# Kernel optimization log

Hardware: AMD Instinct MI355X
Metric: run time of the kernel (lower is better)

The kernel has to match this reference:

```python
import jax, jax.numpy as jnp
import numpy as np

VOCAB, D_EMBED, D_HID = 32000, 512, 512
T, B, S = 64, 32, 256


def setup_inputs() -> dict:
    key = jax.random.key(0)
    ks = jax.random.split(key, 12)
    sE = 1.0 / np.sqrt(D_EMBED)
    sH = 1.0 / np.sqrt(D_HID)
    return {
        "x_seq": jax.random.randint(ks[0], (T, B), 0, VOCAB),
        "h": jax.random.normal(ks[1], (B, D_HID), jnp.float32),
        "c": jax.random.normal(ks[2], (B, D_HID), jnp.float32),
        "context": jax.random.normal(ks[3], (B, S, D_HID), jnp.float32),
        "emb": jax.random.normal(ks[4], (VOCAB, D_EMBED), jnp.float32),
        "W_ih": jax.random.normal(ks[5], (4 * D_HID, D_EMBED), jnp.float32) * sE,
        "W_hh": jax.random.normal(ks[6], (4 * D_HID, D_HID), jnp.float32) * sH,
        "b_ih": jax.random.normal(ks[7], (4 * D_HID,), jnp.float32) * sH,
        "b_hh": jax.random.normal(ks[8], (4 * D_HID,), jnp.float32) * sH,
        "W_attn": jax.random.normal(ks[9], (D_HID, 2 * D_HID), jnp.float32) * sH,
        "W_out": jax.random.normal(ks[10], (VOCAB, D_HID), jnp.float32) * sH,
        "b_out": jax.random.normal(ks[11], (VOCAB,), jnp.float32) * sH,
    }


def reference(x_seq, h, c, context, emb, W_ih, W_hh, b_ih, b_hh, W_attn, W_out, b_out):
    e_seq = emb[x_seq]  # [T, B, E]

    def step(carry, e):
        h, c = carry
        gates = e @ W_ih.T + b_ih + h @ W_hh.T + b_hh  # [B, 4H]
        i, f, g, o = jnp.split(gates, 4, axis=-1)       # torch LSTMCell gate order
        i, f, o = jax.nn.sigmoid(i), jax.nn.sigmoid(f), jax.nn.sigmoid(o)
        g = jnp.tanh(g)
        c = f * c + i * g
        h = o * jnp.tanh(c)
        # dot global attention
        scores = jnp.einsum('bsd,bd->bs', context, h)
        attn = jax.nn.softmax(scores, axis=1)
        wctx = jnp.einsum('bs,bsd->bd', attn, context)
        a = jnp.tanh(jnp.concatenate([h, wctx], axis=1) @ W_attn.T)
        return (h, c), a

    (hf, cf), outs = jax.lax.scan(step, (h, c), e_seq)  # outs: [T, B, H]
    logits = outs.reshape(-1, D_HID) @ W_out.T + b_out   # [T*B, V]
    logp = jax.nn.log_softmax(logits, axis=1).reshape(T, B, VOCAB)
    return logp, hf, cf
```

## Files before the change

kernel.cpp:

```cpp
#include <hip/hip_runtime.h>
#include <hip/hip_cooperative_groups.h>
#include <cstdint>
#include <cstddef>

namespace cg = cooperative_groups;

#define TT 64
#define BB 32
#define SS 256
#define DH 512
#define VV 32000
#define NROWS 2048
#define G4 2048
#define NBLK_SCAN 256
#define NLEAF 32
#define LEAF_TARGET (NBLK_SCAN / NLEAF)

typedef __attribute__((ext_vector_type(8))) short short8;
typedef __attribute__((ext_vector_type(4))) float f32x4;

__device__ __forceinline__ unsigned short f2bf(float x) {
    unsigned u = __float_as_uint(x);
    u += 0x7FFFu + ((u >> 16) & 1u);
    return (unsigned short)(u >> 16);
}
__device__ __forceinline__ float bf2f(unsigned short u) {
    return __uint_as_float((unsigned)u << 16);
}

__device__ __forceinline__ void gload_lds16(const void* g, void* l) {
    __builtin_amdgcn_global_load_lds(
        (const __attribute__((address_space(1))) unsigned int*)g,
        (__attribute__((address_space(3))) unsigned int*)l, 16, 0, 0);
}

__device__ __forceinline__ void coh_store(float* p, float v) {
    __hip_atomic_store(p, v, __ATOMIC_RELAXED, __HIP_MEMORY_SCOPE_AGENT);
}

__global__ void k_convert_bf16(const float* __restrict__ src,
                               unsigned short* __restrict__ dst, int n4) {
    int i = blockIdx.x * blockDim.x + threadIdx.x;
    int stride = gridDim.x * blockDim.x;
    for (; i < n4; i += stride) {
        float4 v = ((const float4*)src)[i];
        ushort4 o;
        o.x = f2bf(v.x); o.y = f2bf(v.y); o.z = f2bf(v.z); o.w = f2bf(v.w);
        ((ushort4*)dst)[i] = o;
    }
}

__global__ void k_convert_hl(const float* __restrict__ src,
                             unsigned short* __restrict__ hi,
                             unsigned short* __restrict__ lo, int n4) {
    int i = blockIdx.x * blockDim.x + threadIdx.x;
    int stride = gridDim.x * blockDim.x;
    for (; i < n4; i += stride) {
        float4 v = ((const float4*)src)[i];
        ushort4 oh, ol;
        float f[4] = {v.x, v.y, v.z, v.w};
        unsigned short h[4], l[4];
#pragma unroll
        for (int e = 0; e < 4; ++e) {
            h[e] = f2bf(f[e]);
            l[e] = f2bf(f[e] - bf2f(h[e]));
        }
        oh.x = h[0]; oh.y = h[1]; oh.z = h[2]; oh.w = h[3];
        ol.x = l[0]; ol.y = l[1]; ol.z = l[2]; ol.w = l[3];
        ((ushort4*)hi)[i] = oh;
        ((ushort4*)lo)[i] = ol;
    }
}

__global__ void k_gather_embed_hl(const int* __restrict__ xseq,
                                  const float* __restrict__ emb,
                                  unsigned short* __restrict__ ehi,
                                  unsigned short* __restrict__ elo,
                                  int* __restrict__ cnt) {
    int gi = blockIdx.x * blockDim.x + threadIdx.x;
    if (gi < TT * NLEAF * 16) cnt[gi] = 0;
    int r = blockIdx.x;
    int tok = xseq[r];
    const float4* s = (const float4*)(emb + (size_t)tok * DH);
    ushort4* dh = (ushort4*)(ehi + (size_t)r * DH);
    ushort4* dl = (ushort4*)(elo + (size_t)r * DH);
    for (int i = threadIdx.x; i < DH / 4; i += blockDim.x) {
        float4 v = s[i];
        float f[4] = {v.x, v.y, v.z, v.w};
        unsigned short h[4], l[4];
#pragma unroll
        for (int e = 0; e < 4; ++e) {
            h[e] = f2bf(f[e]);
            l[e] = f2bf(f[e] - bf2f(h[e]));
        }
        dh[i] = make_ushort4(h[0], h[1], h[2], h[3]);
        dl[i] = make_ushort4(l[0], l[1], l[2], l[3]);
    }
}

__global__ __launch_bounds__(256)
void k_mfma_xpart(const unsigned short* __restrict__ Ahi, const unsigned short* __restrict__ Alo,
                  const unsigned short* __restrict__ Bhi, const unsigned short* __restrict__ Blo,
                  int M, int N, int K,
                  const float* __restrict__ b1, const float* __restrict__ b2,
                  float* __restrict__ Ct) {
    __shared__ unsigned short Ah_s[128 * 64];
    __shared__ unsigned short Al_s[128 * 64];
    __shared__ unsigned short Bh_s[128 * 64];
    __shared__ unsigned short Bl_s[128 * 64];

    const int tid = threadIdx.x;
    const int lane = tid & 63;
    const int wid = tid >> 6;
    const int wm = wid >> 1, wn = wid & 1;
    const int mrow0 = blockIdx.y * 128;
    const int ncol0 = blockIdx.x * 128;
    const int lr = lane & 15;
    const int lk = (lane >> 4) * 8;
    const int rw = (lane >> 4) * 4;

    f32x4 acc[4][4] = {};

    for (int kt = 0; kt < K; kt += 64) {
#pragma unroll
        for (int it = 0; it < 4; ++it) {
            int chunk = it * 256 + tid;
            int r = chunk >> 3;
            int c = (chunk & 7) * 8;
            size_t goA = (size_t)(mrow0 + r) * K + kt + c;
            size_t goB = (size_t)(ncol0 + r) * K + kt + c;
            gload_lds16(Ahi + goA, (void*)(Ah_s + chunk * 8));
            gload_lds16(Alo + goA, (void*)(Al_s + chunk * 8));
            gload_lds16(Bhi + goB, (void*)(Bh_s + chunk * 8));
            gload_lds16(Blo + goB, (void*)(Bl_s + chunk * 8));
        }
        __syncthreads();
#pragma unroll
        for (int kk = 0; kk < 2; ++kk) {
            short8 ah[4], al[4], bh[4], bl[4];
#pragma unroll
            for (int i = 0; i < 4; ++i) {
                int offA = (wm * 64 + i * 16 + lr) * 64 + kk * 32 + lk;
                int offB = (wn * 64 + i * 16 + lr) * 64 + kk * 32 + lk;
                ah[i] = *(const short8*)&Ah_s[offA];
                al[i] = *(const short8*)&Al_s[offA];
                bh[i] = *(const short8*)&Bh_s[offB];
                bl[i] = *(const short8*)&Bl_s[offB];
            }
#pragma unroll
            for (int mi = 0; mi < 4; ++mi)
#pragma unroll
                for (int ni = 0; ni < 4; ++ni) {
                    acc[mi][ni] = __builtin_amdgcn_mfma_f32_16x16x32_bf16(
                        ah[mi], bh[ni], acc[mi][ni], 0, 0, 0);
                    acc[mi][ni] = __builtin_amdgcn_mfma_f32_16x16x32_bf16(
                        ah[mi], bl[ni], acc[mi][ni], 0, 0, 0);
                    acc[mi][ni] = __builtin_amdgcn_mfma_f32_16x16x32_bf16(
                        al[mi], bh[ni], acc[mi][ni], 0, 0, 0);
                }
        }
        __syncthreads();
    }

#pragma unroll
    for (int ni = 0; ni < 4; ++ni) {
        int col = ncol0 + wn * 64 + ni * 16 + lr;
        float bs = b1[col] + b2[col];
#pragma unroll
        for (int mi = 0; mi < 4; ++mi) {
            int grow0 = mrow0 + wm * 64 + mi * 16 + rw;
            float4 o;
            o.x = acc[mi][ni][0] + bs;
            o.y = acc[mi][ni][1] + bs;
            o.z = acc[mi][ni][2] + bs;
            o.w = acc[mi][ni][3] + bs;
            *(float4*)&Ct[(size_t)col * M + grow0] = o;
        }
    }
}

template <int EPI>
__global__ __launch_bounds__(256)
void k_mfma_gemm(const unsigned short* __restrict__ A,
                 const unsigned short* __restrict__ B,
                 int M, int N, int K,
                 const float* __restrict__ bias,
                 float* __restrict__ Cf,
                 unsigned short* __restrict__ Cbf,
                 float* __restrict__ pm, float* __restrict__ ps) {
    __shared__ unsigned short A_s[128 * 64];
    __shared__ unsigned short B_s[128 * 64];
    __shared__ float part_m[2][128];
    __shared__ float part_s[2][128];

    const int tid = threadIdx.x;
    const int lane = tid & 63;
    const int wid = tid >> 6;
    const int wm = wid >> 1, wn = wid & 1;
    const int mrow0 = blockIdx.y * 128;
    const int ncol0 = blockIdx.x * 128;
    const int lr = lane & 15;
    const int lk = (lane >> 4) * 8;
    const int rw = (lane >> 4) * 4;

    f32x4 acc[4][4] = {};

    for (int kt = 0; kt < K; kt += 64) {
#pragma unroll
        for (int it = 0; it < 4; ++it) {
            int chunk = it * 256 + tid;
            int r = chunk >> 3;
            int c = (chunk & 7) * 8;
            gload_lds16(A + (size_t)(mrow0 + r) * K + kt + c, (void*)(A_s + chunk * 8));
            gload_lds16(B + (size_t)(ncol0 + r) * K + kt + c, (void*)(B_s + chunk * 8));
        }
        __syncthreads();
#pragma unroll
        for (int kk = 0; kk < 2; ++kk) {
            short8 afr[4], bfr[4];
#pragma unroll
            for (int i = 0; i < 4; ++i) {
                afr[i] = *(const short8*)&A_s[(wm * 64 + i * 16 + lr) * 64 + kk * 32 + lk];
                bfr[i] = *(const short8*)&B_s[(wn * 64 + i * 16 + lr) * 64 + kk * 32 + lk];
            }
#pragma unroll
            for (int mi = 0; mi < 4; ++mi)
#pragma unroll
                for (int ni = 0; ni < 4; ++ni)
                    acc[mi][ni] = __builtin_amdgcn_mfma_f32_16x16x32_bf16(
                        afr[mi], bfr[ni], acc[mi][ni], 0, 0, 0);
        }
        __syncthreads();
    }

    if constexpr (EPI == 1) {
#pragma unroll
        for (int ni = 0; ni < 4; ++ni) {
            int col = ncol0 + wn * 64 + ni * 16 + lr;
#pragma unroll
            for (int mi = 0; mi < 4; ++mi)
#pragma unroll
                for (int r = 0; r < 4; ++r) {
                    int grow = mrow0 + wm * 64 + mi * 16 + rw + r;
                    Cbf[(size_t)grow * N + col] = f2bf(tanhf(acc[mi][ni][r]));
                }
        }
    } else {
        float bv[4];
#pragma unroll
        for (int ni = 0; ni < 4; ++ni) bv[ni] = bias[ncol0 + wn * 64 + ni * 16 + lr];
#pragma unroll
        for (int mi = 0; mi < 4; ++mi) {
#pragma unroll
            for (int r = 0; r < 4; ++r) {
                int grow = mrow0 + wm * 64 + mi * 16 + rw + r;
                float v[4];
                float mx = -1e30f;
#pragma unroll
                for (int ni = 0; ni < 4; ++ni) {
                    v[ni] = acc[mi][ni][r] + bv[ni];
                    int col = ncol0 + wn * 64 + ni * 16 + lr;
                    Cf[(size_t)grow * N + col] = v[ni];
                    mx = fmaxf(mx, v[ni]);
                }
#pragma unroll
                for (int d = 1; d <= 8; d <<= 1) mx = fmaxf(mx, __shfl_xor(mx, d));
                float ssum = 0.f;
#pragma unroll
                for (int ni = 0; ni < 4; ++ni) ssum += __expf(v[ni] - mx);
#pragma unroll
                for (int d = 1; d <= 8; d <<= 1) ssum += __shfl_xor(ssum, d);
                if (lr == 0) {
                    int lrow = wm * 64 + mi * 16 + rw + r;
                    part_m[wn][lrow] = mx;
                    part_s[wn][lrow] = ssum;
                }
            }
        }
        __syncthreads();
        if (tid < 128) {
            float m0v = part_m[0][tid], m1v = part_m[1][tid];
            float mm = fmaxf(m0v, m1v);
            float ssum = part_s[0][tid] * __expf(m0v - mm) + part_s[1][tid] * __expf(m1v - mm);
            int grow = mrow0 + tid;
            pm[(size_t)grow * gridDim.x + blockIdx.x] = mm;
            ps[(size_t)grow * gridDim.x + blockIdx.x] = ssum;
        }
    }
}

__global__ __launch_bounds__(512, 2)
void k_lstm_scan(const float* __restrict__ xpartT, const float* __restrict__ Whh,
                 const float* __restrict__ h0, const float* __restrict__ c0,
                 float* __restrict__ hTA, float* __restrict__ hTB,
                 float* __restrict__ Hall, unsigned short* __restrict__ catbuf,
                 float* __restrict__ hf, float* __restrict__ cf,
                 int* __restrict__ cnt) {
    __shared__ __align__(16) float h_lds[BB * 8 * 17 * 4];

    const int tid = threadIdx.x;
    const int jl = tid >> 8;
    const int bq = (tid >> 4) & 15;
    const int ks = tid & 15;
    const int jj = blockIdx.x * 2 + jl;

    f32x4 wreg[4][8];
#pragma unroll
    for (int g = 0; g < 4; ++g) {
        const float* wp = Whh + (size_t)(g * DH + jj) * DH + ks * 32;
#pragma unroll
        for (int r = 0; r < 8; ++r)
            wreg[g][r] = *(const f32x4*)(wp + r * 4);
    }

    float creg0 = c0[(size_t)bq * DH + jj];
    float creg1 = c0[(size_t)(bq + 16) * DH + jj];

    float xg0a = 0.f, xg1a = 0.f, xg2a = 0.f, xg3a = 0.f;
    float xg0b = 0.f, xg1b = 0.f, xg2b = 0.f, xg3b = 0.f;
    if (ks == 0) {
        const float* xt = xpartT;
        xg0a = xt[(size_t)(0 * DH + jj) * NROWS + bq];
        xg1a = xt[(size_t)(1 * DH + jj) * NROWS + bq];
        xg2a = xt[(size_t)(2 * DH + jj) * NROWS + bq];
        xg3a = xt[(size_t)(3 * DH + jj) * NROWS + bq];
        xg0b = xt[(size_t)(0 * DH + jj) * NROWS + bq + 16];
        xg1b = xt[(size_t)(1 * DH + jj) * NROWS + bq + 16];
        xg2b = xt[(size_t)(2 * DH + jj) * NROWS + bq + 16];
        xg3b = xt[(size_t)(3 * DH + jj) * NROWS + bq + 16];
    }

    for (int t = 0; t < TT; ++t) {
        const float* hR = (t == 0) ? h0 : ((t & 1) ? hTA : hTB);
        {
            f32x4 v[8];
#pragma unroll
            for (int q = 0; q < 8; ++q)
                asm volatile("global_load_dwordx4 %0, %1, off sc0 sc1"
                             : "=&v"(v[q]) : "v"(hR + (q * 512 + tid) * 4));
            asm volatile("s_waitcnt vmcnt(4)" ::: "memory");
            __builtin_amdgcn_sched_barrier(0);
#pragma unroll
            for (int q = 0; q < 4; ++q) {
                int f = q * 512 + tid;
                int b2 = f >> 7;
                int ks2 = (f & 127) >> 3;
                int r2 = f & 7;
                *(f32x4*)&h_lds[((b2 * 8 + r2) * 17 + ks2) * 4] = v[q];
            }
            asm volatile("s_waitcnt vmcnt(0)" ::: "memory");
            __builtin_amdgcn_sched_barrier(0);
#pragma unroll
            for (int q = 4; q < 8; ++q) {
                int f = q * 512 + tid;
                int b2 = f >> 7;
                int ks2 = (f & 127) >> 3;
                int r2 = f & 7;
                *(f32x4*)&h_lds[((b2 * 8 + r2) * 17 + ks2) * 4] = v[q];
            }
        }
        __syncthreads();

        float a0a = 0.f, a1a = 0.f, a2a = 0.f, a3a = 0.f;
        float a0b = 0.f, a1b = 0.f, a2b = 0.f, a3b = 0.f;
#pragma unroll
        for (int r = 0; r < 8; ++r) {
            f32x4 ha = *(const f32x4*)&h_lds[((bq * 8 + r) * 17 + ks) * 4];
            f32x4 hb = *(const f32x4*)&h_lds[(((bq + 16) * 8 + r) * 17 + ks) * 4];
            a0a += wreg[0][r][0] * ha[0] + wreg[0][r][1] * ha[1]
                 + wreg[0][r][2] * ha[2] + wreg[0][r][3] * ha[3];
            a1a += wreg[1][r][0] * ha[0] + wreg[1][r][1] * ha[1]
                 + wreg[1][r][2] * ha[2] + wreg[1][r][3] * ha[3];
            a2a += wreg[2][r][0] * ha[0] + wreg[2][r][1] * ha[1]
                 + wreg[2][r][2] * ha[2] + wreg[2][r][3] * ha[3];
            a3a += wreg[3][r][0] * ha[0] + wreg[3][r][1] * ha[1]
                 + wreg[3][r][2] * ha[2] + wreg[3][r][3] * ha[3];
            a0b += wreg[0][r][0] * hb[0] + wreg[0][r][1] * hb[1]
                 + wreg[0][r][2] * hb[2] + wreg[0][r][3] * hb[3];
            a1b += wreg[1][r][0] * hb[0] + wreg[1][r][1] * hb[1]
                 + wreg[1][r][2] * hb[2] + wreg[1][r][3] * hb[3];
            a2b += wreg[2][r][0] * hb[0] + wreg[2][r][1] * hb[1]
                 + wreg[2][r][2] * hb[2] + wreg[2][r][3] * hb[3];
            a3b += wreg[3][r][0] * hb[0] + wreg[3][r][1] * hb[1]
                 + wreg[3][r][2] * hb[2] + wreg[3][r][3] * hb[3];
        }
#pragma unroll
        for (int d = 1; d <= 8; d <<= 1) {
            a0a += __shfl_xor(a0a, d); a1a += __shfl_xor(a1a, d);
            a2a += __shfl_xor(a2a, d); a3a += __shfl_xor(a3a, d);
            a0b += __shfl_xor(a0b, d); a1b += __shfl_xor(a1b, d);
            a2b += __shfl_xor(a2b, d); a3b += __shfl_xor(a3b, d);
        }

        if (ks == 0) {
            float* wb = (t & 1) ? hTB : hTA;
#pragma unroll
            for (int bh = 0; bh < 2; ++bh) {
                int b = bh ? bq + 16 : bq;
                float gi = (bh ? a0b : a0a) + (bh ? xg0b : xg0a);
                float gf = (bh ? a1b : a1a) + (bh ? xg1b : xg1a);
                float gg = (bh ? a2b : a2a) + (bh ? xg2b : xg2a);
                float go = (bh ? a3b : a3a) + (bh ? xg3b : xg3a);
                float si = 1.f / (1.f + __expf(-gi));
                float sf = 1.f / (1.f + __expf(-gf));
                float tg = tanhf(gg);
                float so = 1.f / (1.f + __expf(-go));
                float cc = bh ? creg1 : creg0;
                cc = sf * cc + si * tg;
                float hn = so * tanhf(cc);
                if (bh) creg1 = cc; else creg0 = cc;

                coh_store(&wb[(size_t)b * DH + jj], hn);
                int row = t * BB + b;
                Hall[(size_t)row * DH + jj] = hn;
                catbuf[(size_t)row * 1024 + jj] = f2bf(hn);
                if (t == TT - 1) {
                    hf[(size_t)b * DH + jj] = hn;
                    cf[(size_t)b * DH + jj] = cc;
                }
            }
        }

        __syncthreads();
        if (tid == 0) {
            asm volatile("s_waitcnt vmcnt(0)" ::: "memory");
            __hip_atomic_fetch_add(&cnt[t * (NLEAF * 16) + (blockIdx.x & (NLEAF - 1)) * 16], 1,
                                   __ATOMIC_RELAXED, __HIP_MEMORY_SCOPE_AGENT);
        }
        if (ks == 0 && t + 1 < TT) {
            const float* xt = xpartT + (size_t)(t + 1) * BB;
            xg0a = xt[(size_t)(0 * DH + jj) * NROWS + bq];
            xg1a = xt[(size_t)(1 * DH + jj) * NROWS + bq];
            xg2a = xt[(size_t)(2 * DH + jj) * NROWS + bq];
            xg3a = xt[(size_t)(3 * DH + jj) * NROWS + bq];
            xg0b = xt[(size_t)(0 * DH + jj) * NROWS + bq + 16];
            xg1b = xt[(size_t)(1 * DH + jj) * NROWS + bq + 16];
            xg2b = xt[(size_t)(2 * DH + jj) * NROWS + bq + 16];
            xg3b = xt[(size_t)(3 * DH + jj) * NROWS + bq + 16];
        }
        if (tid < NLEAF) {
            while (__hip_atomic_load(&cnt[t * (NLEAF * 16) + tid * 16], __ATOMIC_RELAXED,
                                     __HIP_MEMORY_SCOPE_AGENT) < LEAF_TARGET) {
            }
        }
        __syncthreads();
    }
}

__global__ __launch_bounds__(256)
void k_attn(const float* __restrict__ Hall, const float* __restrict__ ctx,
            unsigned short* __restrict__ catbuf) {
    __shared__ float h4[4][DH];
    __shared__ float p_lds[4][SS];
    __shared__ float l_lds[4];

    const int tid = threadIdx.x;
    const int b = blockIdx.x & 31;
    const int tg = blockIdx.x >> 5;

    for (int i = tid; i < 4 * DH / 4; i += 256) {
        int e = i * 4;
        int ti = e >> 9, k = e & 511;
        float4 v = *(const float4*)(Hall + ((size_t)((tg * 4 + ti) * BB + b)) * DH + k);
        h4[ti][k + 0] = v.x; h4[ti][k + 1] = v.y; h4[ti][k + 2] = v.z; h4[ti][k + 3] = v.w;
    }
    __syncthreads();

    {
        int s = tid;
        float acc[4] = {0.f, 0.f, 0.f, 0.f};
        const float4* cp = (const float4*)(ctx + ((size_t)b * SS + s) * DH);
        for (int kc = 0; kc < DH / 4; ++kc) {
            float4 cv = cp[kc];
#pragma unroll
            for (int i = 0; i < 4; ++i) {
                float4 hv = *(const float4*)&h4[i][kc * 4];
                acc[i] += cv.x * hv.x + cv.y * hv.y + cv.z * hv.z + cv.w * hv.w;
            }
        }
#pragma unroll
        for (int i = 0; i < 4; ++i) p_lds[i][s] = acc[i];
    }
    __syncthreads();

    {
        int w = tid >> 6, l = tid & 63;
        float v0 = p_lds[w][l], v1 = p_lds[w][l + 64];
        float v2 = p_lds[w][l + 128], v3 = p_lds[w][l + 192];
        float mx = fmaxf(fmaxf(v0, v1), fmaxf(v2, v3));
        for (int d = 1; d < 64; d <<= 1) mx = fmaxf(mx, __shfl_xor(mx, d));
        float e0 = __expf(v0 - mx), e1 = __expf(v1 - mx);
        float e2 = __expf(v2 - mx), e3 = __expf(v3 - mx);
        float ssum = e0 + e1 + e2 + e3;
        for (int d = 1; d < 64; d <<= 1) ssum += __shfl_xor(ssum, d);
        p_lds[w][l] = e0; p_lds[w][l + 64] = e1;
        p_lds[w][l + 128] = e2; p_lds[w][l + 192] = e3;
        if (l == 0) l_lds[w] = ssum;
    }
    __syncthreads();

    {
        int d0 = tid * 2;
        float accx[4], accy[4];
#pragma unroll
        for (int i = 0; i < 4; ++i) { accx[i] = 0.f; accy[i] = 0.f; }
        const float* cb = ctx + (size_t)b * SS * DH + d0;
        for (int s = 0; s < SS; ++s) {
            float2 cv = *(const float2*)(cb + (size_t)s * DH);
#pragma unroll
            for (int i = 0; i < 4; ++i) {
                float p = p_lds[i][s];
                accx[i] += p * cv.x;
                accy[i] += p * cv.y;
            }
        }
#pragma unroll
        for (int i = 0; i < 4; ++i) {
            float inv = 1.f / l_lds[i];
            int row = (tg * 4 + i) * BB + b;
            unsigned pack = (unsigned)f2bf(accx[i] * inv) | ((unsigned)f2bf(accy[i] * inv) << 16);
            *(unsigned*)&catbuf[(size_t)row * 1024 + DH + d0] = pack;
        }
    }
}

__global__ __launch_bounds__(256)
void k_lsesub(float* __restrict__ logp, const float* __restrict__ pm,
              const float* __restrict__ ps, int nt) {
    __shared__ float sL;
    const int row = blockIdx.x;
    const int tid = threadIdx.x;
    if (tid < 64) {
        const float* pmr = pm + (size_t)row * nt;
        const float* psr = ps + (size_t)row * nt;
        float m = -1e30f;
        for (int i = tid; i < nt; i += 64) m = fmaxf(m, pmr[i]);
        for (int d = 1; d < 64; d <<= 1) m = fmaxf(m, __shfl_xor(m, d));
        float s = 0.f;
        for (int i = tid; i < nt; i += 64) s += psr[i] * __expf(pmr[i] - m);
        for (int d = 1; d < 64; d <<= 1) s += __shfl_xor(s, d);
        if (tid == 0) sL = m + logf(s);
    }
    __syncthreads();
    float L = sL;
    float4* p = (float4*)(logp + (size_t)row * VV);
    for (int i = tid; i < VV / 4; i += 256) {
        float4 v = p[i];
        v.x -= L; v.y -= L; v.z -= L; v.w -= L;
        p[i] = v;
    }
}

extern "C" void kernel_launch(void* const* d_in, const int* in_sizes, int n_in,
                              void* d_out, int out_size, void* d_ws, size_t ws_size,
                              hipStream_t stream) {
    const int*   xseq  = (const int*)d_in[0];
    const float* h0    = (const float*)d_in[1];
    const float* c0    = (const float*)d_in[2];
    const float* ctx   = (const float*)d_in[3];
    const float* emb   = (const float*)d_in[4];
    const float* Wih   = (const float*)d_in[5];
    const float* Whh   = (const float*)d_in[6];
    const float* bih   = (const float*)d_in[7];
    const float* bhh   = (const float*)d_in[8];
    const float* Wattn = (const float*)d_in[9];
    const float* Wout  = (const float*)d_in[10];
    const float* bout  = (const float*)d_in[11];
    float* out = (float*)d_out;

    char* wptr = (char*)d_ws;
    auto carve = [&](size_t bytes) {
        char* p = wptr;
        wptr += (bytes + 255) & ~(size_t)255;
        return p;
    };
    float*          xpartT  = (float*)carve((size_t)NROWS * G4 * 4);
    float*          Hall    = (float*)carve((size_t)NROWS * DH * 4);
    unsigned short* catbf   = (unsigned short*)carve((size_t)NROWS * 1024 * 2);
    unsigned short* outsbf  = (unsigned short*)carve((size_t)NROWS * DH * 2);
    unsigned short* ehi     = (unsigned short*)carve((size_t)NROWS * DH * 2);
    unsigned short* elo     = (unsigned short*)carve((size_t)NROWS * DH * 2);
    unsigned short* Wihhi   = (unsigned short*)carve((size_t)G4 * DH * 2);
    unsigned short* Wihlo   = (unsigned short*)carve((size_t)G4 * DH * 2);
    unsigned short* Wattnbf = (unsigned short*)carve((size_t)DH * 1024 * 2);
    unsigned short* Woutbf  = (unsigned short*)carve((size_t)VV * DH * 2);
    float*          hTA     = (float*)carve((size_t)BB * DH * 4);
    float*          hTB     = (float*)carve((size_t)BB * DH * 4);
    int*            cnt     = (int*)carve((size_t)TT * NLEAF * 16 * 4);
    float*          pm      = (float*)carve((size_t)NROWS * 250 * 4);
    float*          ps      = (float*)carve((size_t)NROWS * 250 * 4);

    k_convert_bf16<<<256, 256, 0, stream>>>(Wattn, Wattnbf, DH * 1024 / 4);
    k_convert_bf16<<<2048, 256, 0, stream>>>(Wout, Woutbf, VV * DH / 4);
    k_convert_hl<<<512, 256, 0, stream>>>(Wih, Wihhi, Wihlo, G4 * DH / 4);
    k_gather_embed_hl<<<NROWS, 128, 0, stream>>>(xseq, emb, ehi, elo, cnt);

    k_mfma_xpart<<<dim3(16, 16), 256, 0, stream>>>(
        ehi, elo, Wihhi, Wihlo, NROWS, G4, DH, bih, bhh, xpartT);

    {
        const float* a0 = xpartT; const float* a1 = Whh;
        const float* a2 = h0;     const float* a3 = c0;
        float* a4 = hTA; float* a5 = hTB; float* a6 = Hall;
        unsigned short* a7 = catbf;
        float* a8 = out + (size_t)NROWS * VV;
        float* a9 = a8 + BB * DH;
        int* a10 = cnt;
        void* args[] = {&a0, &a1, &a2, &a3, &a4, &a5, &a6, &a7, &a8, &a9, &a10};
        hipLaunchCooperativeKernel((const void*)k_lstm_scan, dim3(NBLK_SCAN), dim3(512),
                                   args, 0, stream);
    }

    k_attn<<<512, 256, 0, stream>>>(Hall, ctx, catbf);

    k_mfma_gemm<1><<<dim3(4, 16), 256, 0, stream>>>(
        catbf, Wattnbf, NROWS, DH, 1024, nullptr, nullptr, outsbf, nullptr, nullptr);

    k_mfma_gemm<2><<<dim3(250, 16), 256, 0, stream>>>(
        outsbf, Woutbf, NROWS, VV, DH, bout, out, nullptr, pm, ps);

    k_lsesub<<<NROWS, 256, 0, stream>>>(out, pm, ps, 250);
}
```

Baseline: 853.6 us.

## Store logits as bf16 intermediate and swizzle output-GEMM block order

The vocab-projection GEMM now writes bf16 logits to a workspace buffer instead of fp32 into the output, and the log-softmax subtraction kernel reads that bf16 data and writes fp32 results. This halves the GEMM's store traffic and replaces the read-modify-write of fp32 output with a bf16 read. It also linearizes the grid and swizzles block indices so neighbouring blocks share W_out/activation tiles for better L2 reuse. Logits are rounded to bf16 before the max-subtraction, which costs accuracy, and the path depends on the workspace being large enough.

```diff
diff --git a/kernel.cpp b/kernel.cpp
--- a/kernel.cpp
+++ b/kernel.cpp
@@ -15,8 +15,11 @@
 #define NBLK_SCAN 256
 #define NLEAF 32
 #define LEAF_TARGET (NBLK_SCAN / NLEAF)
+#define NTILE_N 250
+#define NTILE_M 16
 
 typedef __attribute__((ext_vector_type(8))) short short8;
+typedef __attribute__((ext_vector_type(8))) unsigned short ushort8v;
 typedef __attribute__((ext_vector_type(4))) float f32x4;
 
 __device__ __forceinline__ unsigned short f2bf(float x) {
@@ -197,8 +200,18 @@
     const int lane = tid & 63;
     const int wid = tid >> 6;
     const int wm = wid >> 1, wn = wid & 1;
-    const int mrow0 = blockIdx.y * 128;
-    const int ncol0 = blockIdx.x * 128;
+
+    int bx, by;
+    if constexpr (EPI >= 2) {
+        int lin = blockIdx.x;
+        int swz = (lin & 7) * 500 + (lin >> 3);
+        by = swz / NTILE_N;
+        bx = swz - by * NTILE_N;
+    } else {
+        bx = blockIdx.x; by = blockIdx.y;
+    }
+    const int mrow0 = by * 128;
+    const int ncol0 = bx * 128;
     const int lr = lane & 15;
     const int lk = (lane >> 4) * 8;
     const int rw = (lane >> 4) * 4;
@@ -260,7 +273,10 @@
                 for (int ni = 0; ni < 4; ++ni) {
                     v[ni] = acc[mi][ni][r] + bv[ni];
                     int col = ncol0 + wn * 64 + ni * 16 + lr;
-                    Cf[(size_t)grow * N + col] = v[ni];
+                    if constexpr (EPI == 3)
+                        Cbf[(size_t)grow * N + col] = f2bf(v[ni]);
+                    else
+                        Cf[(size_t)grow * N + col] = v[ni];
                     mx = fmaxf(mx, v[ni]);
                 }
 #pragma unroll
@@ -283,8 +299,8 @@
             float mm = fmaxf(m0v, m1v);
             float ssum = part_s[0][tid] * __expf(m0v - mm) + part_s[1][tid] * __expf(m1v - mm);
             int grow = mrow0 + tid;
-            pm[(size_t)grow * gridDim.x + blockIdx.x] = mm;
-            ps[(size_t)grow * gridDim.x + blockIdx.x] = ssum;
+            pm[(size_t)grow * NTILE_N + bx] = mm;
+            ps[(size_t)grow * NTILE_N + bx] = ssum;
         }
     }
 }
@@ -524,9 +540,10 @@
     }
 }
 
+template <bool BF16IN>
 __global__ __launch_bounds__(256)
-void k_lsesub(float* __restrict__ logp, const float* __restrict__ pm,
-              const float* __restrict__ ps, int nt) {
+void k_lsesub(float* __restrict__ logp, const unsigned short* __restrict__ Lbf,
+              const float* __restrict__ pm, const float* __restrict__ ps, int nt) {
     __shared__ float sL;
     const int row = blockIdx.x;
     const int tid = threadIdx.x;
@@ -543,11 +560,30 @@
     }
     __syncthreads();
     float L = sL;
-    float4* p = (float4*)(logp + (size_t)row * VV);
-    for (int i = tid; i < VV / 4; i += 256) {
-        float4 v = p[i];
-        v.x -= L; v.y -= L; v.z -= L; v.w -= L;
-        p[i] = v;
+    if constexpr (BF16IN) {
+        const ushort8v* src = (const ushort8v*)(Lbf + (size_t)row * VV);
+        float4* dst = (float4*)(logp + (size_t)row * VV);
+        for (int i = tid; i < VV / 8; i += 256) {
+            ushort8v v = src[i];
+            float4 o0, o1;
+            o0.x = bf2f((unsigned short)v[0]) - L;
+            o0.y = bf2f((unsigned short)v[1]) - L;
+            o0.z = bf2f((unsigned short)v[2]) - L;
+            o0.w = bf2f((unsigned short)v[3]) - L;
+            o1.x = bf2f((unsigned short)v[4]) - L;
+            o1.y = bf2f((unsigned short)v[5]) - L;
+            o1.z = bf2f((unsigned short)v[6]) - L;
+            o1.w = bf2f((unsigned short)v[7]) - L;
+            dst[i * 2] = o0;
+            dst[i * 2 + 1] = o1;
+        }
+    } else {
+        float4* p = (float4*)(logp + (size_t)row * VV);
+        for (int i = tid; i < VV / 4; i += 256) {
+            float4 v = p[i];
+            v.x -= L; v.y -= L; v.z -= L; v.w -= L;
+            p[i] = v;
+        }
     }
 }
 
@@ -587,8 +623,12 @@
     float*          hTA     = (float*)carve((size_t)BB * DH * 4);
     float*          hTB     = (float*)carve((size_t)BB * DH * 4);
     int*            cnt     = (int*)carve((size_t)TT * NLEAF * 16 * 4);
-    float*          pm      = (float*)carve((size_t)NROWS * 250 * 4);
-    float*          ps      = (float*)carve((size_t)NROWS * 250 * 4);
+    float*          pm      = (float*)carve((size_t)NROWS * NTILE_N * 4);
+    float*          ps      = (float*)carve((size_t)NROWS * NTILE_N * 4);
+    char* mark = wptr;
+    unsigned short* Lbf = (unsigned short*)carve((size_t)NROWS * VV * 2);
+    bool use_bf16_logits = ((size_t)(wptr - (char*)d_ws) <= ws_size);
+    if (!use_bf16_logits) { wptr = mark; Lbf = nullptr; }
 
     k_convert_bf16<<<256, 256, 0, stream>>>(Wattn, Wattnbf, DH * 1024 / 4);
     k_convert_bf16<<<2048, 256, 0, stream>>>(Wout, Woutbf, VV * DH / 4);
@@ -616,8 +656,13 @@
     k_mfma_gemm<1><<<dim3(4, 16), 256, 0, stream>>>(
         catbf, Wattnbf, NROWS, DH, 1024, nullptr, nullptr, outsbf, nullptr, nullptr);
 
-    k_mfma_gemm<2><<<dim3(250, 16), 256, 0, stream>>>(
-        outsbf, Woutbf, NROWS, VV, DH, bout, out, nullptr, pm, ps);
-
-    k_lsesub<<<NROWS, 256, 0, stream>>>(out, pm, ps, 250);
-}
+    if (use_bf16_logits) {
+        k_mfma_gemm<3><<<NTILE_N * NTILE_M, 256, 0, stream>>>(
+            outsbf, Woutbf, NROWS, VV, DH, bout, nullptr, Lbf, pm, ps);
+        k_lsesub<true><<<NROWS, 256, 0, stream>>>(out, Lbf, pm, ps, NTILE_N);
+    } else {
+        k_mfma_gemm<2><<<NTILE_N * NTILE_M, 256, 0, stream>>>(
+            outsbf, Woutbf, NROWS, VV, DH, bout, out, nullptr, pm, ps);
+        k_lsesub<false><<<NROWS, 256, 0, stream>>>(out, nullptr, pm, ps, NTILE_N);
+    }
+}
```

New measurement: 834.5 us. 2.2% less time.
